# Optimization experiments

Measured on AMD Instinct MI355X. Metric: run time of the kernel, lower is better.

The kernel has to match this reference:

```python
import jax, jax.numpy as jnp
import numpy as np

LAMBDA_COOR = 5.0
LAMBDA_NOOBJ = 0.5


def setup_inputs() -> dict:
    key = jax.random.key(0)
    k1, k2 = jax.random.split(key)
    B, W, H, C = 128, 256, 256, 5
    outputs = jax.random.normal(k1, (B, W, H, C), dtype=jnp.float32)
    targets = jax.random.normal(k2, (B, W, H, C), dtype=jnp.float32)
    return {"outputs": outputs, "targets": targets}


def reference(outputs, targets):
    # channel layout per cell: (conf, x, y, w, h)
    conf_pred = outputs[..., 0]
    conf_gt = targets[..., 0]
    obj_mask = conf_gt > 0
    # sum of squared coord errors (x, y, w, h) per cell: [B, W, H]
    coord_sq = jnp.sum((outputs[..., 1:] - targets[..., 1:]) ** 2, axis=-1)
    obj_loss = LAMBDA_COOR * coord_sq + (conf_pred - 1.0) ** 2
    noobj_loss = LAMBDA_NOOBJ * conf_pred ** 2
    loss = jnp.sum(jnp.where(obj_mask, obj_loss, noobj_loss))
    return loss / outputs.shape[0]
```

## Files before the change

### kernel.cpp

```cpp
#include <hip/hip_runtime.h>

#define LAMBDA_COOR 5.0f
#define LAMBDA_NOOBJ 0.5f

__global__ __launch_bounds__(256, 4) void yolo_loss_kernel(
    const float* __restrict__ outp, const float* __restrict__ tgt,
    float* __restrict__ loss, int n_groups, float inv_b)
{
    const int tid = blockIdx.x * blockDim.x + threadIdx.x;
    const int nth = gridDim.x * blockDim.x;
    float acc = 0.0f;

    for (int g0 = tid * 4; g0 < n_groups; g0 += nth * 4) {
        if (g0 + 4 <= n_groups) {
            #pragma unroll 1
            for (int it = 0; it < 2; ++it) {
                const float4* o4 = (const float4*)(outp + (size_t)(g0 + 2 * it) * 20);
                const float4* t4 = (const float4*)(tgt  + (size_t)(g0 + 2 * it) * 20);
                float4 ov[10], tv[10];
                #pragma unroll
                for (int i = 0; i < 10; ++i) ov[i] = o4[i];
                #pragma unroll
                for (int i = 0; i < 10; ++i) tv[i] = t4[i];

                float of[40], tf[40];
                #pragma unroll
                for (int i = 0; i < 10; ++i) {
                    of[4*i+0] = ov[i].x; of[4*i+1] = ov[i].y;
                    of[4*i+2] = ov[i].z; of[4*i+3] = ov[i].w;
                    tf[4*i+0] = tv[i].x; tf[4*i+1] = tv[i].y;
                    tf[4*i+2] = tv[i].z; tf[4*i+3] = tv[i].w;
                }

                #pragma unroll
                for (int c = 0; c < 8; ++c) {
                    float cp = of[5*c];
                    float cg = tf[5*c];
                    float coord = 0.0f;
                    #pragma unroll
                    for (int k = 1; k < 5; ++k) {
                        float d = of[5*c + k] - tf[5*c + k];
                        coord = fmaf(d, d, coord);
                    }
                    float dm1 = cp - 1.0f;
                    float obj = fmaf(LAMBDA_COOR, coord, dm1 * dm1);
                    float nob = LAMBDA_NOOBJ * cp * cp;
                    acc += (cg > 0.0f) ? obj : nob;
                }
            }
        } else {
            for (int g = g0; g < n_groups; ++g) {
                const float4* o4 = (const float4*)(outp + (size_t)g * 20);
                const float4* t4 = (const float4*)(tgt  + (size_t)g * 20);
                float o[20], t[20];
                #pragma unroll
                for (int i = 0; i < 5; ++i) {
                    float4 a = o4[i];
                    float4 b = t4[i];
                    o[4*i+0] = a.x; o[4*i+1] = a.y; o[4*i+2] = a.z; o[4*i+3] = a.w;
                    t[4*i+0] = b.x; t[4*i+1] = b.y; t[4*i+2] = b.z; t[4*i+3] = b.w;
                }
                #pragma unroll
                for (int c = 0; c < 4; ++c) {
                    float cp = o[5*c];
                    float cg = t[5*c];
                    float coord = 0.0f;
                    #pragma unroll
                    for (int k = 1; k < 5; ++k) {
                        float d = o[5*c + k] - t[5*c + k];
                        coord = fmaf(d, d, coord);
                    }
                    float dm1 = cp - 1.0f;
                    float obj = fmaf(LAMBDA_COOR, coord, dm1 * dm1);
                    float nob = LAMBDA_NOOBJ * cp * cp;
                    acc += (cg > 0.0f) ? obj : nob;
                }
            }
        }
    }

    #pragma unroll
    for (int off = 32; off > 0; off >>= 1)
        acc += __shfl_down(acc, off, 64);

    __shared__ float wave_sums[4];
    int lane = threadIdx.x & 63;
    int wid  = threadIdx.x >> 6;
    if (lane == 0) wave_sums[wid] = acc;
    __syncthreads();

    if (threadIdx.x == 0) {
        float s = wave_sums[0] + wave_sums[1] + wave_sums[2] + wave_sums[3];
        atomicAdd(loss, s * inv_b);
    }
}

extern "C" void kernel_launch(void* const* d_in, const int* in_sizes, int n_in,
                              void* d_out, int out_size, void* d_ws, size_t ws_size,
                              hipStream_t stream) {
    const float* outputs = (const float*)d_in[0];
    const float* targets = (const float*)d_in[1];
    float* loss = (float*)d_out;

    const int n_elems  = in_sizes[0];
    const int n_groups = n_elems / 20;
    const float inv_b  = 1.0f / 128.0f;

    hipMemsetAsync(d_out, 0, sizeof(float), stream);

    const int threads = 256;
    const int blocks  = 2048;
    yolo_loss_kernel<<<blocks, threads, 0, stream>>>(
        outputs, targets, loss, n_groups, inv_b);
}
```

Measured before the change: 394.5 us.

## Stage inputs through LDS with async global_load_lds double buffering per wave

Replaces per-thread strided float4 loads with fully coalesced per-wave global-to-LDS direct loads (global_load_lds). Each wave double-buffers a 64-group chunk and uses explicit vmcnt waits so the next chunk's loads overlap with compute on the current one. The aim is to fix the uncoalesced 80-byte-stride access pattern and keep memory in flight. The grid shrinks from 2048 to 512 blocks. The kernel now uses 80 KB of LDS per block, which limits occupancy, and correctness depends on the hand-written waitcnt ordering.

```diff
diff --git a/kernel.cpp b/kernel.cpp
--- a/kernel.cpp
+++ b/kernel.cpp
@@ -1,80 +1,117 @@
 #include <hip/hip_runtime.h>
+#include <stdint.h>
 
 #define LAMBDA_COOR 5.0f
 #define LAMBDA_NOOBJ 0.5f
 
-__global__ __launch_bounds__(256, 4) void yolo_loss_kernel(
+
+typedef __attribute__((address_space(3))) uint8_t as3_t;
+typedef __attribute__((address_space(1))) uint8_t as1_t;
+
+__device__ __forceinline__ void gload16(const void* gptr, void* lptr) {
+    __builtin_amdgcn_global_load_lds((const as1_t*)gptr, (as3_t*)lptr, 16, 0, 0);
+}
+
+__global__ __launch_bounds__(256) void yolo_loss_kernel(
     const float* __restrict__ outp, const float* __restrict__ tgt,
     float* __restrict__ loss, int n_groups, float inv_b)
 {
-    const int tid = blockIdx.x * blockDim.x + threadIdx.x;
-    const int nth = gridDim.x * blockDim.x;
+    __shared__ float lds[4][2][2][1280];
+
+    const int lane = threadIdx.x & 63;
+    const int wid  = threadIdx.x >> 6;
+    const int W    = blockIdx.x * 4 + wid;
+    const int NW   = gridDim.x * 4;
+
+    const int F = n_groups >> 6;
+    const int m = (W < F) ? ((F - 1 - W) / NW + 1) : 0;
+
+    const float4* o4 = (const float4*)outp;
+    const float4* t4 = (const float4*)tgt;
+
     float acc = 0.0f;
 
-    for (int g0 = tid * 4; g0 < n_groups; g0 += nth * 4) {
-        if (g0 + 4 <= n_groups) {
-            #pragma unroll 1
-            for (int it = 0; it < 2; ++it) {
-                const float4* o4 = (const float4*)(outp + (size_t)(g0 + 2 * it) * 20);
-                const float4* t4 = (const float4*)(tgt  + (size_t)(g0 + 2 * it) * 20);
-                float4 ov[10], tv[10];
+    auto issue = [&](int j, int slot) {
+        const long cb = ((long)W + (long)j * NW) * 320;
+        float* lo = &lds[wid][slot][0][0];
+        float* lt = &lds[wid][slot][1][0];
+        #pragma unroll
+        for (int k = 0; k < 5; ++k)
+            gload16(o4 + cb + k * 64 + lane, lo + k * 256);
+        #pragma unroll
+        for (int k = 0; k < 5; ++k)
+            gload16(t4 + cb + k * 64 + lane, lt + k * 256);
+    };
+
+    if (m > 0) issue(0, 0);
+    if (m > 1) issue(1, 1);
+
+    #pragma unroll 1
+    for (int j = 0; j < m; ++j) {
+        const int s = j & 1;
+        if (j + 1 < m) { asm volatile("s_waitcnt vmcnt(10)" ::: "memory"); }
+        else           { asm volatile("s_waitcnt vmcnt(0)"  ::: "memory"); }
+        __builtin_amdgcn_sched_barrier(0);
+
+        const float4* po = (const float4*)&lds[wid][s][0][lane * 20];
+        const float4* pt = (const float4*)&lds[wid][s][1][lane * 20];
+        float o[20], t[20];
+        #pragma unroll
+        for (int i = 0; i < 5; ++i) {
+            float4 a = po[i], b = pt[i];
+            o[4*i+0] = a.x; o[4*i+1] = a.y; o[4*i+2] = a.z; o[4*i+3] = a.w;
+            t[4*i+0] = b.x; t[4*i+1] = b.y; t[4*i+2] = b.z; t[4*i+3] = b.w;
+        }
+        #pragma unroll
+        for (int c = 0; c < 4; ++c) {
+            float cp = o[5*c];
+            float cg = t[5*c];
+            float coord = 0.0f;
+            #pragma unroll
+            for (int k = 1; k < 5; ++k) {
+                float d = o[5*c + k] - t[5*c + k];
+                coord = fmaf(d, d, coord);
+            }
+            float dm1 = cp - 1.0f;
+            float obj = fmaf(LAMBDA_COOR, coord, dm1 * dm1);
+            float nob = LAMBDA_NOOBJ * cp * cp;
+            acc += (cg > 0.0f) ? obj : nob;
+        }
+
+        if (j + 2 < m) {
+            asm volatile("s_waitcnt lgkmcnt(0)" ::: "memory");
+            __builtin_amdgcn_sched_barrier(0);
+            issue(j + 2, s);
+        }
+    }
+
+    {
+        const int gstart = F << 6;
+        const int gtid   = blockIdx.x * blockDim.x + threadIdx.x;
+        const int nth    = gridDim.x * blockDim.x;
+        for (int g = gstart + gtid; g < n_groups; g += nth) {
+            const float4* og = (const float4*)(outp + (size_t)g * 20);
+            const float4* tg = (const float4*)(tgt  + (size_t)g * 20);
+            float o[20], t[20];
+            #pragma unroll
+            for (int i = 0; i < 5; ++i) {
+                float4 a = og[i], b = tg[i];
+                o[4*i+0] = a.x; o[4*i+1] = a.y; o[4*i+2] = a.z; o[4*i+3] = a.w;
+                t[4*i+0] = b.x; t[4*i+1] = b.y; t[4*i+2] = b.z; t[4*i+3] = b.w;
+            }
+            #pragma unroll
+            for (int c = 0; c < 4; ++c) {
+                float cp = o[5*c], cg = t[5*c];
+                float coord = 0.0f;
                 #pragma unroll
-                for (int i = 0; i < 10; ++i) ov[i] = o4[i];
-                #pragma unroll
-                for (int i = 0; i < 10; ++i) tv[i] = t4[i];
-
-                float of[40], tf[40];
-                #pragma unroll
-                for (int i = 0; i < 10; ++i) {
-                    of[4*i+0] = ov[i].x; of[4*i+1] = ov[i].y;
-                    of[4*i+2] = ov[i].z; of[4*i+3] = ov[i].w;
-                    tf[4*i+0] = tv[i].x; tf[4*i+1] = tv[i].y;
-                    tf[4*i+2] = tv[i].z; tf[4*i+3] = tv[i].w;
+                for (int k = 1; k < 5; ++k) {
+                    float d = o[5*c + k] - t[5*c + k];
+                    coord = fmaf(d, d, coord);
                 }
-
-                #pragma unroll
-                for (int c = 0; c < 8; ++c) {
-                    float cp = of[5*c];
-                    float cg = tf[5*c];
-                    float coord = 0.0f;
-                    #pragma unroll
-                    for (int k = 1; k < 5; ++k) {
-                        float d = of[5*c + k] - tf[5*c + k];
-                        coord = fmaf(d, d, coord);
-                    }
-                    float dm1 = cp - 1.0f;
-                    float obj = fmaf(LAMBDA_COOR, coord, dm1 * dm1);
-                    float nob = LAMBDA_NOOBJ * cp * cp;
-                    acc += (cg > 0.0f) ? obj : nob;
-                }
-            }
-        } else {
-            for (int g = g0; g < n_groups; ++g) {
-                const float4* o4 = (const float4*)(outp + (size_t)g * 20);
-                const float4* t4 = (const float4*)(tgt  + (size_t)g * 20);
-                float o[20], t[20];
-                #pragma unroll
-                for (int i = 0; i < 5; ++i) {
-                    float4 a = o4[i];
-                    float4 b = t4[i];
-                    o[4*i+0] = a.x; o[4*i+1] = a.y; o[4*i+2] = a.z; o[4*i+3] = a.w;
-                    t[4*i+0] = b.x; t[4*i+1] = b.y; t[4*i+2] = b.z; t[4*i+3] = b.w;
-                }
-                #pragma unroll
-                for (int c = 0; c < 4; ++c) {
-                    float cp = o[5*c];
-                    float cg = t[5*c];
-                    float coord = 0.0f;
-                    #pragma unroll
-                    for (int k = 1; k < 5; ++k) {
-                        float d = o[5*c + k] - t[5*c + k];
-                        coord = fmaf(d, d, coord);
-                    }
-                    float dm1 = cp - 1.0f;
-                    float obj = fmaf(LAMBDA_COOR, coord, dm1 * dm1);
-                    float nob = LAMBDA_NOOBJ * cp * cp;
-                    acc += (cg > 0.0f) ? obj : nob;
-                }
+                float dm1 = cp - 1.0f;
+                float obj = fmaf(LAMBDA_COOR, coord, dm1 * dm1);
+                float nob = LAMBDA_NOOBJ * cp * cp;
+                acc += (cg > 0.0f) ? obj : nob;
             }
         }
     }
@@ -84,8 +121,6 @@
         acc += __shfl_down(acc, off, 64);
 
     __shared__ float wave_sums[4];
-    int lane = threadIdx.x & 63;
-    int wid  = threadIdx.x >> 6;
     if (lane == 0) wave_sums[wid] = acc;
     __syncthreads();
 
@@ -109,7 +144,7 @@
     hipMemsetAsync(d_out, 0, sizeof(float), stream);
 
     const int threads = 256;
-    const int blocks  = 2048;
+    const int blocks  = 512;
     yolo_loss_kernel<<<blocks, threads, 0, stream>>>(
         outputs, targets, loss, n_groups, inv_b);
 }
```

Result: faster. 332.4 us (-15.7%).
